# Kernel optimization log

Hardware: AMD Instinct MI355X
Metric: run time of the kernel (lower is better)

## Reference

```python
import jax, jax.numpy as jnp
import numpy as np

HID = 64
EPS = 1e-12  # tf.contrib.layers.layer_norm variance_epsilon


def _ln(x, g, b):
    m = jnp.mean(x, axis=-1, keepdims=True)
    v = jnp.mean(jnp.square(x - m), axis=-1, keepdims=True)
    return (x - m) * jax.lax.rsqrt(v + EPS) * g + b


def setup_inputs() -> dict:
    key = jax.random.key(0)
    k1, k2, k3, k4 = jax.random.split(key, 4)
    N, T, OBS, ACT = 2048, 256, 96, 32
    D = OBS + ACT
    obss = jax.random.normal(k1, (N, T, OBS), dtype=jnp.float32)
    actions = jax.random.normal(k2, (N, T, ACT), dtype=jnp.float32)
    W = jax.random.normal(k3, (D + HID, 4 * HID), dtype=jnp.float32) * (1.0 / np.sqrt(D + HID))
    ln_gamma = jnp.ones((5, HID), dtype=jnp.float32)   # i, j, f, o, state norms
    ln_beta = jnp.zeros((5, HID), dtype=jnp.float32)
    dense_W = jax.random.uniform(k4, (HID, 1), dtype=jnp.float32, minval=-0.003, maxval=0.003)
    dense_b = jnp.zeros((1,), dtype=jnp.float32)
    return {"obss": obss, "actions": actions, "W": W, "ln_gamma": ln_gamma,
            "ln_beta": ln_beta, "dense_W": dense_W, "dense_b": dense_b}


def reference(obss, actions, W, ln_gamma, ln_beta, dense_W, dense_b):
    # [N,T,obs+act] -> time-major [T,N,D]
    x = jnp.concatenate([obss, actions], axis=-1)
    xt = jnp.transpose(x, (1, 0, 2))
    N = x.shape[0]
    c0 = jnp.zeros((N, HID), dtype=x.dtype)
    h0 = jnp.zeros((N, HID), dtype=x.dtype)
    forget_bias = jnp.asarray(1.0, dtype=x.dtype)

    def step(carry, x_t):
        c, h = carry
        z = jnp.concatenate([x_t, h], axis=-1) @ W  # [N, 4*HID], no bias
        i, j, f, o = jnp.split(z, 4, axis=-1)
        i = _ln(i, ln_gamma[0], ln_beta[0])
        j = _ln(j, ln_gamma[1], ln_beta[1])
        f = _ln(f, ln_gamma[2], ln_beta[2])
        o = _ln(o, ln_gamma[3], ln_beta[3])
        new_c = c * jax.nn.sigmoid(f + forget_bias) + jax.nn.sigmoid(i) * jnp.tanh(j)
        new_c = _ln(new_c, ln_gamma[4], ln_beta[4])
        new_h = jnp.tanh(new_c) * jax.nn.sigmoid(o)
        return (new_c, new_h), new_h

    _, hs = jax.lax.scan(step, (c0, h0), xt)  # hs: [T,N,HID]
    outputs = jnp.transpose(hs, (1, 0, 2))     # [N,T,HID]
    q = outputs @ dense_W + dense_b            # [N,T,1]
    return q
```

## Files before the change

kernel.cpp:

```cpp
#include <hip/hip_runtime.h>

#define TT 256
#define OBS 96
#define ACTD 32
#define RPB 16
#define XCS 136
#define HS 72
#define ZS 68
#define EPS 1e-12f

typedef __bf16 bf16x8 __attribute__((ext_vector_type(8)));
typedef float f32x4 __attribute__((ext_vector_type(4)));
typedef unsigned short u16x8 __attribute__((ext_vector_type(8)));
typedef unsigned int u32;
typedef unsigned short u16;

__device__ __forceinline__ u16 f2bf(float f) {
  u32 x = __builtin_bit_cast(u32, f);
  x += 0x7fffu + ((x >> 16) & 1u);
  return (u16)(x >> 16);
}
__device__ __forceinline__ u32 pk2bf(float a, float b) {
  return (u32)f2bf(a) | ((u32)f2bf(b) << 16);
}
__device__ __forceinline__ float sigm(float x) { return 1.0f / (1.0f + __expf(-x)); }
__device__ __forceinline__ float tanh_(float x) { return 1.0f - 2.0f / (__expf(2.0f * x) + 1.0f); }

template <int CTRL>
__device__ __forceinline__ float dpp_add(float x) {
  int t = __builtin_amdgcn_update_dpp(0, __builtin_bit_cast(int, x), CTRL, 0xF, 0xF, true);
  return x + __builtin_bit_cast(float, t);
}
__device__ __forceinline__ float red16(float x) {
  x = dpp_add<0xB1>(x);
  x = dpp_add<0x4E>(x);
  x = dpp_add<0x124>(x);
  x = dpp_add<0x128>(x);
  return x;
}

__global__ __launch_bounds__(512, 2) void lstm_fused(
    const float* __restrict__ obss, const float* __restrict__ actions,
    const float* __restrict__ Wm, const float* __restrict__ gamma,
    const float* __restrict__ beta, const float* __restrict__ dWv,
    const float* __restrict__ dbv, float* __restrict__ out)
{
  __shared__ u16 xchunk[8][RPB][XCS];
  __shared__ u16 hbuf[RPB][HS];
  __shared__ float zbuf[4][RPB][ZS];
  __shared__ float pbuf[4][RPB][2][2];
  __shared__ float qbuf[RPB][8];

  const int tid = threadIdx.x;
  const int wv = tid >> 6;
  const int ln = tid & 63;
  const int l15 = ln & 15;
  const int quad = ln >> 4;
  const int g = wv & 3;
  const int half = wv >> 2;
  const int n0 = blockIdx.x * RPB;

  for (int i = tid; i < RPB * HS / 2; i += 512) ((u32*)hbuf)[i] = 0u;

  u16x8 bw[6][2];
  #pragma unroll
  for (int kt = 0; kt < 6; ++kt)
    #pragma unroll
    for (int nt = 0; nt < 2; ++nt)
      #pragma unroll
      for (int j = 0; j < 8; ++j)
        bw[kt][nt][j] =
            f2bf(Wm[(kt * 32 + quad * 8 + j) * 256 + g * 64 + half * 32 + nt * 16 + l15]);

  const int crow = (wv & 3) * 4 + quad;
  const int c0 = l15 * 4;
  float ggam[4][4], gbet[4][4], cgam[4], cbet[4], dwv[4];
  #pragma unroll
  for (int e = 0; e < 4; ++e) {
    cgam[e] = gamma[4 * 64 + c0 + e];
    cbet[e] = beta[4 * 64 + c0 + e];
    dwv[e] = dWv[c0 + e];
    #pragma unroll
    for (int gg = 0; gg < 4; ++gg) {
      ggam[gg][e] = gamma[gg * 64 + c0 + e];
      gbet[gg][e] = beta[gg * 64 + c0 + e];
    }
  }
  const float bias = dbv[0];

  const int srow = tid >> 5;
  const int slot = tid & 31;
  const float* obs_p = obss + (size_t)(n0 + srow) * TT * OBS;
  const float* act_p = actions + (size_t)(n0 + srow) * TT * ACTD;

  f32x4 xst[8];
  #pragma unroll
  for (int s = 0; s < 8; ++s) {
    int tl = s;
    xst[s] = (slot < 24) ? *(const f32x4*)(obs_p + tl * OBS + slot * 4)
                         : *(const f32x4*)(act_p + tl * ACTD + (slot - 24) * 4);
  }
  #pragma unroll
  for (int s = 0; s < 8; ++s)
    *(uint2*)&xchunk[s][srow][slot * 4] =
        make_uint2(pk2bf(xst[s][0], xst[s][1]), pk2bf(xst[s][2], xst[s][3]));

  f32x4 cst = {0.0f, 0.0f, 0.0f, 0.0f};
  __syncthreads();

  for (int t = 0; t < TT; ++t) {
    const int tm = t & 7;

    if (tm == 0) {
      #pragma unroll
      for (int s = 0; s < 8; ++s) {
        int tl = t + 8 + s; if (tl > TT - 1) tl = TT - 1;
        xst[s] = (slot < 24) ? *(const f32x4*)(obs_p + tl * OBS + slot * 4)
                             : *(const f32x4*)(act_p + tl * ACTD + (slot - 24) * 4);
      }
      if (t > 0 && wv >= 4 && wv < 6) {
        const int j = tid - 256;
        const int row = j >> 3, tt = j & 7;
        out[(size_t)(n0 + row) * TT + (t - 8) + tt] = qbuf[row][tt] + bias;
      }
    }

    u16x8 af[6];
    #pragma unroll
    for (int kt = 0; kt < 4; ++kt)
      af[kt] = *(const u16x8*)&xchunk[tm][l15][kt * 32 + quad * 8];
    #pragma unroll
    for (int kt = 4; kt < 6; ++kt)
      af[kt] = *(const u16x8*)&hbuf[l15][(kt - 4) * 32 + quad * 8];

    f32x4 acc0 = {0.0f, 0.0f, 0.0f, 0.0f}, acc1 = acc0;
    #pragma unroll
    for (int kt = 0; kt < 6; ++kt) {
      acc0 = __builtin_amdgcn_mfma_f32_16x16x32_bf16(
          __builtin_bit_cast(bf16x8, af[kt]), __builtin_bit_cast(bf16x8, bw[kt][0]), acc0, 0, 0, 0);
      acc1 = __builtin_amdgcn_mfma_f32_16x16x32_bf16(
          __builtin_bit_cast(bf16x8, af[kt]), __builtin_bit_cast(bf16x8, bw[kt][1]), acc1, 0, 0, 0);
    }

    float s[4], ss[4];
    #pragma unroll
    for (int r = 0; r < 4; ++r) {
      s[r]  = acc0[r] + acc1[r];
      ss[r] = acc0[r] * acc0[r] + acc1[r] * acc1[r];
      s[r]  = red16(s[r]);
      ss[r] = red16(ss[r]);
    }
    #pragma unroll
    for (int r = 0; r < 4; ++r) {
      const int row = quad * 4 + r;
      zbuf[g][row][half * 32 + l15]      = acc0[r];
      zbuf[g][row][half * 32 + 16 + l15] = acc1[r];
    }
    if (l15 < 4) {
      const float sv  = l15 == 0 ? s[0]  : l15 == 1 ? s[1]  : l15 == 2 ? s[2]  : s[3];
      const float ssv = l15 == 0 ? ss[0] : l15 == 1 ? ss[1] : l15 == 2 ? ss[2] : ss[3];
      *(float2*)&pbuf[g][quad * 4 + l15][half][0] = make_float2(sv, ssv);
    }
    __syncthreads();

    if (wv < 4) {
      float zc[4][4];
      #pragma unroll
      for (int gg = 0; gg < 4; ++gg) {
        const f32x4 p = *(const f32x4*)&pbuf[gg][crow][0][0];
        const float mean = (p[0] + p[2]) * (1.0f / 64.0f);
        const float var  = (p[1] + p[3]) * (1.0f / 64.0f) - mean * mean;
        const float rstd = rsqrtf(var + EPS);
        const f32x4 z = *(const f32x4*)&zbuf[gg][crow][c0];
        #pragma unroll
        for (int e = 0; e < 4; ++e)
          zc[gg][e] = (z[e] - mean) * rstd * ggam[gg][e] + gbet[gg][e];
      }
      float nc[4];
      #pragma unroll
      for (int e = 0; e < 4; ++e)
        nc[e] = cst[e] * sigm(zc[2][e] + 1.0f) + sigm(zc[0][e]) * tanh_(zc[1][e]);
      float s2  = red16(nc[0] + nc[1] + nc[2] + nc[3]);
      float ss2 = red16(nc[0] * nc[0] + nc[1] * nc[1] + nc[2] * nc[2] + nc[3] * nc[3]);
      const float mean = s2 * (1.0f / 64.0f);
      const float var  = ss2 * (1.0f / 64.0f) - mean * mean;
      const float rstd = rsqrtf(var + EPS);
      float h[4];
      #pragma unroll
      for (int e = 0; e < 4; ++e) {
        const float cn = (nc[e] - mean) * rstd * cgam[e] + cbet[e];
        cst[e] = cn;
        h[e] = tanh_(cn) * sigm(zc[3][e]);
      }
      *(uint2*)&hbuf[crow][c0] = make_uint2(pk2bf(h[0], h[1]), pk2bf(h[2], h[3]));
      float qp = red16(h[0] * dwv[0] + h[1] * dwv[1] + h[2] * dwv[2] + h[3] * dwv[3]);
      if (l15 == 0) qbuf[crow][tm] = qp;
    }
    if (tm == 7) {
      #pragma unroll
      for (int s = 0; s < 8; ++s)
        *(uint2*)&xchunk[s][srow][slot * 4] =
            make_uint2(pk2bf(xst[s][0], xst[s][1]), pk2bf(xst[s][2], xst[s][3]));
    }
    __syncthreads();
  }

  if (wv >= 4 && wv < 6) {
    const int j = tid - 256;
    const int row = j >> 3, tt = j & 7;
    out[(size_t)(n0 + row) * TT + 248 + tt] = qbuf[row][tt] + bias;
  }
}

extern "C" void kernel_launch(void* const* d_in, const int* in_sizes, int n_in,
                              void* d_out, int out_size, void* d_ws, size_t ws_size,
                              hipStream_t stream) {
  const float* obss    = (const float*)d_in[0];
  const float* actions = (const float*)d_in[1];
  const float* Wm      = (const float*)d_in[2];
  const float* gamma   = (const float*)d_in[3];
  const float* beta    = (const float*)d_in[4];
  const float* dWv     = (const float*)d_in[5];
  const float* dbv     = (const float*)d_in[6];
  float* out = (float*)d_out;
  lstm_fused<<<dim3(2048 / RPB), dim3(512), 0, stream>>>(obss, actions, Wm, gamma,
                                                         beta, dWv, dbv, out);
}
```

Before: 697.0 us.

## Halve rows per block, precompute chunked input projection, spread cell update across all waves

Rows per block drop from 16 to 8, doubling the grid to 256 blocks so more CUs get work. The input-projection MFMAs for 8 timesteps are batched at each chunk start and stored as fp16 in shared memory, leaving only the h-projection MFMAs on the serial per-step path. The cell/LN update now uses all 8 waves, one row per wave and one unit per lane, with 64-wide reductions through shuffles. Precision moves from bf16 to fp16, and half of each 16-row MFMA tile is wasted since only 8 rows are real.

```diff
diff --git a/kernel.cpp b/kernel.cpp
--- a/kernel.cpp
+++ b/kernel.cpp
@@ -3,25 +3,30 @@
 #define TT 256
 #define OBS 96
 #define ACTD 32
-#define RPB 16
+#define RPB 8
+#define CH 8
 #define XCS 136
-#define HS 72
-#define ZS 68
+#define ZXS 12
+#define ZBS 69
 #define EPS 1e-12f
 
-typedef __bf16 bf16x8 __attribute__((ext_vector_type(8)));
+typedef _Float16 f16x8 __attribute__((ext_vector_type(8)));
 typedef float f32x4 __attribute__((ext_vector_type(4)));
 typedef unsigned short u16x8 __attribute__((ext_vector_type(8)));
 typedef unsigned int u32;
 typedef unsigned short u16;
 
-__device__ __forceinline__ u16 f2bf(float f) {
-  u32 x = __builtin_bit_cast(u32, f);
-  x += 0x7fffu + ((x >> 16) & 1u);
-  return (u16)(x >> 16);
-}
-__device__ __forceinline__ u32 pk2bf(float a, float b) {
-  return (u32)f2bf(a) | ((u32)f2bf(b) << 16);
+__device__ __forceinline__ u16 f2h(float f) {
+  return __builtin_bit_cast(u16, (_Float16)f);
+}
+__device__ __forceinline__ u32 pk2h(float a, float b) {
+  return (u32)f2h(a) | ((u32)f2h(b) << 16);
+}
+__device__ __forceinline__ float h2f_lo(u32 v) {
+  return (float)__builtin_bit_cast(_Float16, (u16)(v & 0xffffu));
+}
+__device__ __forceinline__ float h2f_hi(u32 v) {
+  return (float)__builtin_bit_cast(_Float16, (u16)(v >> 16));
 }
 __device__ __forceinline__ float sigm(float x) { return 1.0f / (1.0f + __expf(-x)); }
 __device__ __forceinline__ float tanh_(float x) { return 1.0f - 2.0f / (__expf(2.0f * x) + 1.0f); }
@@ -38,6 +43,12 @@
   x = dpp_add<0x128>(x);
   return x;
 }
+__device__ __forceinline__ float red64(float x) {
+  x = red16(x);
+  x += __shfl_xor(x, 16, 64);
+  x += __shfl_xor(x, 32, 64);
+  return x;
+}
 
 __global__ __launch_bounds__(512, 2) void lstm_fused(
     const float* __restrict__ obss, const float* __restrict__ actions,
@@ -45,11 +56,12 @@
     const float* __restrict__ beta, const float* __restrict__ dWv,
     const float* __restrict__ dbv, float* __restrict__ out)
 {
-  __shared__ u16 xchunk[8][RPB][XCS];
-  __shared__ u16 hbuf[RPB][HS];
-  __shared__ float zbuf[4][RPB][ZS];
-  __shared__ float pbuf[4][RPB][2][2];
-  __shared__ float qbuf[RPB][8];
+  __shared__ u16 xchunk[CH][RPB][XCS];
+  __shared__ u16 zxT[CH][256][ZXS];
+  __shared__ float zbuf[4][16][ZBS];
+  __shared__ float pbuf[4][16][4];
+  __shared__ u16 hbuf[RPB][72];
+  __shared__ float qbuf[CH][RPB];
 
   const int tid = threadIdx.x;
   const int wv = tid >> 6;
@@ -59,8 +71,9 @@
   const int g = wv & 3;
   const int half = wv >> 2;
   const int n0 = blockIdx.x * RPB;
-
-  for (int i = tid; i < RPB * HS / 2; i += 512) ((u32*)hbuf)[i] = 0u;
+  const int c0 = g * 64 + half * 32 + l15;
+
+  for (int i = tid; i < RPB * 72 / 2; i += 512) ((u32*)hbuf)[i] = 0u;
 
   u16x8 bw[6][2];
   #pragma unroll
@@ -69,146 +82,153 @@
     for (int nt = 0; nt < 2; ++nt)
       #pragma unroll
       for (int j = 0; j < 8; ++j)
-        bw[kt][nt][j] =
-            f2bf(Wm[(kt * 32 + quad * 8 + j) * 256 + g * 64 + half * 32 + nt * 16 + l15]);
-
-  const int crow = (wv & 3) * 4 + quad;
-  const int c0 = l15 * 4;
-  float ggam[4][4], gbet[4][4], cgam[4], cbet[4], dwv[4];
-  #pragma unroll
-  for (int e = 0; e < 4; ++e) {
-    cgam[e] = gamma[4 * 64 + c0 + e];
-    cbet[e] = beta[4 * 64 + c0 + e];
-    dwv[e] = dWv[c0 + e];
-    #pragma unroll
-    for (int gg = 0; gg < 4; ++gg) {
-      ggam[gg][e] = gamma[gg * 64 + c0 + e];
-      gbet[gg][e] = beta[gg * 64 + c0 + e];
-    }
-  }
+        bw[kt][nt][j] = f2h(Wm[(kt * 32 + quad * 8 + j) * 256 + c0 + nt * 16]);
+
+  float ggam[4], gbet[4];
+  #pragma unroll
+  for (int gg = 0; gg < 4; ++gg) {
+    ggam[gg] = gamma[gg * 64 + ln];
+    gbet[gg] = beta[gg * 64 + ln];
+  }
+  const float cgam = gamma[4 * 64 + ln], cbet = beta[4 * 64 + ln];
+  const float dw = dWv[ln];
   const float bias = dbv[0];
 
-  const int srow = tid >> 5;
+  const int sp = tid >> 8;
+  const int srow = (tid >> 5) & 7;
   const int slot = tid & 31;
   const float* obs_p = obss + (size_t)(n0 + srow) * TT * OBS;
   const float* act_p = actions + (size_t)(n0 + srow) * TT * ACTD;
 
-  f32x4 xst[8];
-  #pragma unroll
-  for (int s = 0; s < 8; ++s) {
-    int tl = s;
-    xst[s] = (slot < 24) ? *(const f32x4*)(obs_p + tl * OBS + slot * 4)
-                         : *(const f32x4*)(act_p + tl * ACTD + (slot - 24) * 4);
-  }
-  #pragma unroll
-  for (int s = 0; s < 8; ++s)
+  f32x4 xst[4];
+  #pragma unroll
+  for (int k = 0; k < 4; ++k) {
+    const int s = sp + 2 * k;
+    xst[k] = (slot < 24) ? *(const f32x4*)(obs_p + s * OBS + slot * 4)
+                         : *(const f32x4*)(act_p + s * ACTD + (slot - 24) * 4);
+  }
+  #pragma unroll
+  for (int k = 0; k < 4; ++k) {
+    const int s = sp + 2 * k;
     *(uint2*)&xchunk[s][srow][slot * 4] =
-        make_uint2(pk2bf(xst[s][0], xst[s][1]), pk2bf(xst[s][2], xst[s][3]));
-
-  f32x4 cst = {0.0f, 0.0f, 0.0f, 0.0f};
+        make_uint2(pk2h(xst[k][0], xst[k][1]), pk2h(xst[k][2], xst[k][3]));
+  }
+
+  float creg = 0.0f;
   __syncthreads();
 
   for (int t = 0; t < TT; ++t) {
     const int tm = t & 7;
 
     if (tm == 0) {
-      #pragma unroll
-      for (int s = 0; s < 8; ++s) {
-        int tl = t + 8 + s; if (tl > TT - 1) tl = TT - 1;
-        xst[s] = (slot < 24) ? *(const f32x4*)(obs_p + tl * OBS + slot * 4)
+      if (t > 0 && tid < 64) {
+        const int s = tid >> 3, row = tid & 7;
+        out[(size_t)(n0 + row) * TT + (t - 8) + s] = qbuf[s][row] + bias;
+      }
+      #pragma unroll
+      for (int k = 0; k < 4; ++k) {
+        int tl = t + 8 + sp + 2 * k; if (tl > TT - 1) tl = TT - 1;
+        xst[k] = (slot < 24) ? *(const f32x4*)(obs_p + tl * OBS + slot * 4)
                              : *(const f32x4*)(act_p + tl * ACTD + (slot - 24) * 4);
       }
-      if (t > 0 && wv >= 4 && wv < 6) {
-        const int j = tid - 256;
-        const int row = j >> 3, tt = j & 7;
-        out[(size_t)(n0 + row) * TT + (t - 8) + tt] = qbuf[row][tt] + bias;
-      }
-    }
-
-    u16x8 af[6];
-    #pragma unroll
-    for (int kt = 0; kt < 4; ++kt)
-      af[kt] = *(const u16x8*)&xchunk[tm][l15][kt * 32 + quad * 8];
-    #pragma unroll
-    for (int kt = 4; kt < 6; ++kt)
-      af[kt] = *(const u16x8*)&hbuf[l15][(kt - 4) * 32 + quad * 8];
-
-    f32x4 acc0 = {0.0f, 0.0f, 0.0f, 0.0f}, acc1 = acc0;
-    #pragma unroll
-    for (int kt = 0; kt < 6; ++kt) {
-      acc0 = __builtin_amdgcn_mfma_f32_16x16x32_bf16(
-          __builtin_bit_cast(bf16x8, af[kt]), __builtin_bit_cast(bf16x8, bw[kt][0]), acc0, 0, 0, 0);
-      acc1 = __builtin_amdgcn_mfma_f32_16x16x32_bf16(
-          __builtin_bit_cast(bf16x8, af[kt]), __builtin_bit_cast(bf16x8, bw[kt][1]), acc1, 0, 0, 0);
+      #pragma unroll
+      for (int s = 0; s < CH; ++s) {
+        u16x8 afx[4];
+        #pragma unroll
+        for (int kt = 0; kt < 4; ++kt)
+          afx[kt] = *(const u16x8*)&xchunk[s][l15 & 7][kt * 32 + quad * 8];
+        f32x4 ax0 = {0.f, 0.f, 0.f, 0.f}, ax1 = ax0;
+        #pragma unroll
+        for (int kt = 0; kt < 4; ++kt) {
+          ax0 = __builtin_amdgcn_mfma_f32_16x16x32_f16(
+              __builtin_bit_cast(f16x8, afx[kt]), __builtin_bit_cast(f16x8, bw[kt][0]), ax0, 0, 0, 0);
+          ax1 = __builtin_amdgcn_mfma_f32_16x16x32_f16(
+              __builtin_bit_cast(f16x8, afx[kt]), __builtin_bit_cast(f16x8, bw[kt][1]), ax1, 0, 0, 0);
+        }
+        if (quad < 2) {
+          *(uint2*)&zxT[s][c0][quad * 4] =
+              make_uint2(pk2h(ax0[0], ax0[1]), pk2h(ax0[2], ax0[3]));
+          *(uint2*)&zxT[s][c0 + 16][quad * 4] =
+              make_uint2(pk2h(ax1[0], ax1[1]), pk2h(ax1[2], ax1[3]));
+        }
+      }
+    }
+
+    const u16x8 afh0 = *(const u16x8*)&hbuf[l15 & 7][quad * 8];
+    const u16x8 afh1 = *(const u16x8*)&hbuf[l15 & 7][32 + quad * 8];
+    f32x4 acc0 = {0.f, 0.f, 0.f, 0.f}, acc1 = acc0;
+    acc0 = __builtin_amdgcn_mfma_f32_16x16x32_f16(
+        __builtin_bit_cast(f16x8, afh0), __builtin_bit_cast(f16x8, bw[4][0]), acc0, 0, 0, 0);
+    acc1 = __builtin_amdgcn_mfma_f32_16x16x32_f16(
+        __builtin_bit_cast(f16x8, afh0), __builtin_bit_cast(f16x8, bw[4][1]), acc1, 0, 0, 0);
+    acc0 = __builtin_amdgcn_mfma_f32_16x16x32_f16(
+        __builtin_bit_cast(f16x8, afh1), __builtin_bit_cast(f16x8, bw[5][0]), acc0, 0, 0, 0);
+    acc1 = __builtin_amdgcn_mfma_f32_16x16x32_f16(
+        __builtin_bit_cast(f16x8, afh1), __builtin_bit_cast(f16x8, bw[5][1]), acc1, 0, 0, 0);
+
+    {
+      const uint2 zx0 = *(const uint2*)&zxT[tm][c0][(quad & 1) * 4];
+      const uint2 zx1 = *(const uint2*)&zxT[tm][c0 + 16][(quad & 1) * 4];
+      acc0[0] += h2f_lo(zx0.x); acc0[1] += h2f_hi(zx0.x);
+      acc0[2] += h2f_lo(zx0.y); acc0[3] += h2f_hi(zx0.y);
+      acc1[0] += h2f_lo(zx1.x); acc1[1] += h2f_hi(zx1.x);
+      acc1[2] += h2f_lo(zx1.y); acc1[3] += h2f_hi(zx1.y);
     }
 
     float s[4], ss[4];
     #pragma unroll
     for (int r = 0; r < 4; ++r) {
-      s[r]  = acc0[r] + acc1[r];
-      ss[r] = acc0[r] * acc0[r] + acc1[r] * acc1[r];
-      s[r]  = red16(s[r]);
-      ss[r] = red16(ss[r]);
+      s[r]  = red16(acc0[r] + acc1[r]);
+      ss[r] = red16(acc0[r] * acc0[r] + acc1[r] * acc1[r]);
     }
     #pragma unroll
     for (int r = 0; r < 4; ++r) {
-      const int row = quad * 4 + r;
-      zbuf[g][row][half * 32 + l15]      = acc0[r];
-      zbuf[g][row][half * 32 + 16 + l15] = acc1[r];
+      zbuf[g][quad * 4 + r][half * 32 + l15]      = acc0[r];
+      zbuf[g][quad * 4 + r][half * 32 + 16 + l15] = acc1[r];
     }
     if (l15 < 4) {
       const float sv  = l15 == 0 ? s[0]  : l15 == 1 ? s[1]  : l15 == 2 ? s[2]  : s[3];
       const float ssv = l15 == 0 ? ss[0] : l15 == 1 ? ss[1] : l15 == 2 ? ss[2] : ss[3];
-      *(float2*)&pbuf[g][quad * 4 + l15][half][0] = make_float2(sv, ssv);
+      *(float2*)&pbuf[g][quad * 4 + l15][half * 2] = make_float2(sv, ssv);
     }
     __syncthreads();
 
-    if (wv < 4) {
-      float zc[4][4];
-      #pragma unroll
-      for (int gg = 0; gg < 4; ++gg) {
-        const f32x4 p = *(const f32x4*)&pbuf[gg][crow][0][0];
-        const float mean = (p[0] + p[2]) * (1.0f / 64.0f);
-        const float var  = (p[1] + p[3]) * (1.0f / 64.0f) - mean * mean;
-        const float rstd = rsqrtf(var + EPS);
-        const f32x4 z = *(const f32x4*)&zbuf[gg][crow][c0];
-        #pragma unroll
-        for (int e = 0; e < 4; ++e)
-          zc[gg][e] = (z[e] - mean) * rstd * ggam[gg][e] + gbet[gg][e];
-      }
-      float nc[4];
-      #pragma unroll
-      for (int e = 0; e < 4; ++e)
-        nc[e] = cst[e] * sigm(zc[2][e] + 1.0f) + sigm(zc[0][e]) * tanh_(zc[1][e]);
-      float s2  = red16(nc[0] + nc[1] + nc[2] + nc[3]);
-      float ss2 = red16(nc[0] * nc[0] + nc[1] * nc[1] + nc[2] * nc[2] + nc[3] * nc[3]);
-      const float mean = s2 * (1.0f / 64.0f);
-      const float var  = ss2 * (1.0f / 64.0f) - mean * mean;
+    float zc[4];
+    #pragma unroll
+    for (int gg = 0; gg < 4; ++gg) {
+      const f32x4 p = *(const f32x4*)&pbuf[gg][wv][0];
+      const float mean = (p[0] + p[2]) * (1.0f / 64.0f);
+      const float var  = (p[1] + p[3]) * (1.0f / 64.0f) - mean * mean;
       const float rstd = rsqrtf(var + EPS);
-      float h[4];
-      #pragma unroll
-      for (int e = 0; e < 4; ++e) {
-        const float cn = (nc[e] - mean) * rstd * cgam[e] + cbet[e];
-        cst[e] = cn;
-        h[e] = tanh_(cn) * sigm(zc[3][e]);
-      }
-      *(uint2*)&hbuf[crow][c0] = make_uint2(pk2bf(h[0], h[1]), pk2bf(h[2], h[3]));
-      float qp = red16(h[0] * dwv[0] + h[1] * dwv[1] + h[2] * dwv[2] + h[3] * dwv[3]);
-      if (l15 == 0) qbuf[crow][tm] = qp;
-    }
+      zc[gg] = (zbuf[gg][wv][ln] - mean) * rstd * ggam[gg] + gbet[gg];
+    }
+    const float nc = creg * sigm(zc[2] + 1.0f) + sigm(zc[0]) * tanh_(zc[1]);
+    const float s2  = red64(nc);
+    const float ss2 = red64(nc * nc);
+    const float mean = s2 * (1.0f / 64.0f);
+    const float var  = ss2 * (1.0f / 64.0f) - mean * mean;
+    const float rstd = rsqrtf(var + EPS);
+    const float cn = (nc - mean) * rstd * cgam + cbet;
+    creg = cn;
+    const float h = tanh_(cn) * sigm(zc[3]);
+    hbuf[wv][ln] = f2h(h);
+    const float qp = red64(h * dw);
+    if (ln == 0) qbuf[tm][wv] = qp;
+
     if (tm == 7) {
       #pragma unroll
-      for (int s = 0; s < 8; ++s)
-        *(uint2*)&xchunk[s][srow][slot * 4] =
-            make_uint2(pk2bf(xst[s][0], xst[s][1]), pk2bf(xst[s][2], xst[s][3]));
+      for (int k = 0; k < 4; ++k) {
+        const int scm = sp + 2 * k;
+        *(uint2*)&xchunk[scm][srow][slot * 4] =
+            make_uint2(pk2h(xst[k][0], xst[k][1]), pk2h(xst[k][2], xst[k][3]));
+      }
     }
     __syncthreads();
   }
 
-  if (wv >= 4 && wv < 6) {
-    const int j = tid - 256;
-    const int row = j >> 3, tt = j & 7;
-    out[(size_t)(n0 + row) * TT + 248 + tt] = qbuf[row][tt] + bias;
+  if (tid < 64) {
+    const int s = tid >> 3, row = tid & 7;
+    out[(size_t)(n0 + row) * TT + 248 + s] = qbuf[s][row] + bias;
   }
 }
 
```

After: 666.4 us. 1.05x faster.
